# Kernel optimization log

Hardware: AMD Instinct MI355X
Metric: run time of the kernel (lower is better)

The kernel has to match this reference:

```python
import jax, jax.numpy as jnp
import numpy as np

B, S, HID, NH = 2, 2048, 2048, 16
HD = HID // NH  # 128


def setup_inputs() -> dict:
    key = jax.random.key(0)
    ks = jax.random.split(key, 6)
    xav = lambda k, shape: jax.random.uniform(k, shape, jnp.float32,
        -jnp.sqrt(6.0 / (shape[0] + shape[1])), jnp.sqrt(6.0 / (shape[0] + shape[1])))
    return {
        'hidden_state': jax.random.normal(ks[0], (B, S, HID), jnp.float32),
        'attention_mask': jnp.ones((B, 1, 1, S), jnp.int32),
        'Wq': xav(ks[1], (HID, HID)), 'bq': jnp.zeros((HID,), jnp.float32),
        'Wk': xav(ks[2], (HD, HID)),  'bk': jnp.zeros((HD,), jnp.float32),
        'Wv': xav(ks[3], (HD, HID)),  'bv': jnp.zeros((HD,), jnp.float32),
        'Wo': xav(ks[4], (HID, HID)), 'bo': jnp.zeros((HID,), jnp.float32),
    }


def reference(hidden_state, attention_mask, Wq, bq, Wk, bk, Wv, bv, Wo, bo):
    b, s, _ = hidden_state.shape
    scale = 1.0 / jnp.sqrt(jnp.float32(HD))
    # projections (torch Linear: y = x @ W.T + b)
    q = hidden_state @ Wq.T + bq                      # (B,S,HID)
    k = hidden_state @ Wk.T + bk                      # (B,S,HD) single KV head
    v = hidden_state @ Wv.T + bv                      # (B,S,HD)
    q = q.reshape(b, s, NH, HD).transpose(0, 2, 1, 3)  # (B,H,S,D)
    # scores with shared KV head broadcast over query heads
    scores = jnp.einsum('bhqd,bkd->bhqk', q, k) * scale  # (B,H,S,S)
    scores = jnp.where(attention_mask == 0, -jnp.inf, scores)
    probs = jax.nn.softmax(scores, axis=-1)
    out = jnp.einsum('bhqk,bkd->bhqd', probs, v)       # (B,H,S,D)
    out = out.transpose(0, 2, 1, 3).reshape(b, s, HID)
    return out @ Wo.T + bo
```

## Files before the change

kernel.cpp:

```cpp
#include <hip/hip_runtime.h>

#define B_   2
#define S_   2048
#define HID_ 2048
#define NH_  16
#define HD_  128
#define M_   (B_ * S_)

using half4   = __attribute__((ext_vector_type(4))) _Float16;
using half8   = __attribute__((ext_vector_type(8))) _Float16;
using floatx4 = __attribute__((ext_vector_type(4))) float;

__device__ __forceinline__ void gl_lds16(const void* g, void* l) {
  __builtin_amdgcn_global_load_lds(
      (const __attribute__((address_space(1))) void*)g,
      (__attribute__((address_space(3))) void*)l, 16, 0, 0);
}

__device__ __forceinline__ void cvt8(const float* s, _Float16* d, int i) {
  const floatx4* sp = (const floatx4*)s;
  floatx4 a = sp[(size_t)i * 2];
  floatx4 b = sp[(size_t)i * 2 + 1];
  half8 h;
  h[0] = (_Float16)a[0]; h[1] = (_Float16)a[1];
  h[2] = (_Float16)a[2]; h[3] = (_Float16)a[3];
  h[4] = (_Float16)b[0]; h[5] = (_Float16)b[1];
  h[6] = (_Float16)b[2]; h[7] = (_Float16)b[3];
  *(half8*)(d + (size_t)i * 8) = h;
}

__global__ __launch_bounds__(256) void cvt_all(
    const float* __restrict__ h,  const float* __restrict__ wq,
    const float* __restrict__ wk, const float* __restrict__ wv,
    const float* __restrict__ wo,
    _Float16* __restrict__ dh,  _Float16* __restrict__ dwq,
    _Float16* __restrict__ dwk, _Float16* __restrict__ dwv,
    _Float16* __restrict__ dwo) {
  int bid = blockIdx.x;
  const float* s;
  _Float16* d;
  int off;
  if (bid < 4096)      { s = h;  d = dh;  off = bid; }
  else if (bid < 6144) { s = wq; d = dwq; off = bid - 4096; }
  else if (bid < 6272) { s = wk; d = dwk; off = bid - 6144; }
  else if (bid < 6400) { s = wv; d = dwv; off = bid - 6272; }
  else                 { s = wo; d = dwo; off = bid - 6400; }
  cvt8(s, d, off * 256 + threadIdx.x);
}

template <typename OutT, bool TRANS>
__device__ __forceinline__ void gemm128_body(
    const _Float16* __restrict__ A, const _Float16* __restrict__ W,
    const float* __restrict__ bias, OutT* __restrict__ C,
    int Nout, int K, int m0, int n0w, int c0) {
  __shared__ __align__(16) _Float16 As[128][32];
  __shared__ __align__(16) _Float16 Ws[128][32];

  const int tid  = threadIdx.x;
  const int lane = tid & 63;
  const int wave = tid >> 6;
  const int wm   = wave >> 1, wn = wave & 1;
  const int l15  = lane & 15, lq = lane >> 4;
  const int srow = wave * 16 + (lane >> 2);
  const int scol = (lane & 3) * 8;

  floatx4 acc[4][4];
#pragma unroll
  for (int i = 0; i < 4; i++)
#pragma unroll
    for (int j = 0; j < 4; j++) acc[i][j] = (floatx4){0.f, 0.f, 0.f, 0.f};

  const _Float16* Ag = A + (size_t)(m0 + srow) * K + scol;
  const _Float16* Wg = W + (size_t)(n0w + srow) * K + scol;
  const size_t step64 = (size_t)64 * K;

  for (int kt = 0; kt < K; kt += 32) {
    gl_lds16(Ag + kt,          &As[wave * 16][0]);
    gl_lds16(Ag + step64 + kt, &As[64 + wave * 16][0]);
    gl_lds16(Wg + kt,          &Ws[wave * 16][0]);
    gl_lds16(Wg + step64 + kt, &Ws[64 + wave * 16][0]);
    __syncthreads();

    half8 af[4], bf[4];
#pragma unroll
    for (int i = 0; i < 4; i++)
      af[i] = *(const half8*)&As[wm * 64 + i * 16 + l15][lq * 8];
#pragma unroll
    for (int j = 0; j < 4; j++)
      bf[j] = *(const half8*)&Ws[wn * 64 + j * 16 + l15][lq * 8];
#pragma unroll
    for (int i = 0; i < 4; i++)
#pragma unroll
      for (int j = 0; j < 4; j++)
        acc[i][j] = __builtin_amdgcn_mfma_f32_16x16x32_f16(af[i], bf[j], acc[i][j], 0, 0, 0);
    __syncthreads();
  }

  const int rq = lq * 4;
  if constexpr (TRANS) {
    const int b  = m0 / S_;
    const int sb = m0 - b * S_ + wm * 64;
#pragma unroll
    for (int j = 0; j < 4; j++) {
      int col  = wn * 64 + j * 16 + l15;
      float bv = bias[n0w + col];
#pragma unroll
      for (int i = 0; i < 4; i++) {
        half4 o;
#pragma unroll
        for (int r = 0; r < 4; r++) o[r] = (_Float16)(acc[i][j][r] + bv);
        *(half4*)((_Float16*)C + (size_t)b * HD_ * S_ + (size_t)col * S_
                  + sb + i * 16 + rq) = o;
      }
    }
  } else {
#pragma unroll
    for (int j = 0; j < 4; j++) {
      int col_l = wn * 64 + j * 16 + l15;
      float bv  = bias[n0w + col_l];
#pragma unroll
      for (int i = 0; i < 4; i++) {
        int row = m0 + wm * 64 + i * 16 + rq;
#pragma unroll
        for (int r = 0; r < 4; r++)
          C[(size_t)(row + r) * Nout + c0 + col_l] = (OutT)(acc[i][j][r] + bv);
      }
    }
  }
}

__global__ __launch_bounds__(256) void gemm_qkv(
    const _Float16* __restrict__ A,
    const _Float16* __restrict__ Wq, const float* __restrict__ bq, _Float16* __restrict__ Qh,
    const _Float16* __restrict__ Wk, const float* __restrict__ bk, _Float16* __restrict__ Kh,
    const _Float16* __restrict__ Wv, const float* __restrict__ bv, _Float16* __restrict__ VhT) {
  const int nt = blockIdx.x, m0 = blockIdx.y * 128;
  if (nt < 16)
    gemm128_body<_Float16, false>(A, Wq, bq, Qh, HID_, HID_, m0, nt * 128, nt * 128);
  else if (nt == 16)
    gemm128_body<_Float16, false>(A, Wk, bk, Kh, HD_, HID_, m0, 0, 0);
  else
    gemm128_body<_Float16, true>(A, Wv, bv, VhT, HD_, HID_, m0, 0, 0);
}

__global__ __launch_bounds__(256) void gemm_out(
    const _Float16* __restrict__ A, const _Float16* __restrict__ W,
    const float* __restrict__ bias, float* __restrict__ C) {
  gemm128_body<float, false>(A, W, bias, C, HID_, HID_, blockIdx.y * 128,
                             blockIdx.x * 128, blockIdx.x * 128);
}

__global__ __launch_bounds__(256, 2) void attn_mfma(
    const _Float16* __restrict__ Q, const _Float16* __restrict__ K,
    const _Float16* __restrict__ VhT, const int* __restrict__ mask,
    _Float16* __restrict__ Obuf) {
  constexpr int BN = 64, KP = 136, VP = 72, NT = S_ / BN;
  __shared__ __align__(16) _Float16 Ks[2][BN][KP];
  __shared__ __align__(16) _Float16 Vt[2][HD_][VP];

  const int tid  = threadIdx.x;
  const int lane = tid & 63, wave = tid >> 6;
  const int l15  = lane & 15, lq = lane >> 4;
  const int q0   = blockIdx.x * 128;
  const int b    = blockIdx.y >> 4, h = blockIdx.y & 15;
  const float sl2e = 0.08838834764831845f * 1.44269504088896341f;
  const _Float16* VT = VhT + (size_t)b * HD_ * S_;
  const _Float16* Kb = K + (size_t)b * S_ * HD_;
  const int* mb = mask + b * S_;

  int krow[4], kcol[4], vrow[4], vcol[4];
#pragma unroll
  for (int it = 0; it < 4; it++) {
    int i = it * 256 + tid;
    krow[it] = i >> 4;  kcol[it] = (i & 15) * 8;
    vrow[it] = i >> 3;  vcol[it] = (i & 7) * 8;
  }

  half8 qf[2][4];
#pragma unroll
  for (int i = 0; i < 2; i++)
#pragma unroll
    for (int kd = 0; kd < 4; kd++)
      qf[i][kd] = *(const half8*)(Q + (size_t)(b * S_ + q0 + wave * 32 + i * 16 + l15) * HID_
                                  + h * HD_ + kd * 32 + lq * 8);

  float m_i[2] = {-3.0e38f, -3.0e38f};
  float l_p[2] = {0.f, 0.f};
  floatx4 oacc[2][8];
#pragma unroll
  for (int i = 0; i < 2; i++)
#pragma unroll
    for (int jd = 0; jd < 8; jd++) oacc[i][jd] = (floatx4){0.f, 0.f, 0.f, 0.f};

  half8 kreg[4], vreg[4];
#pragma unroll
  for (int it = 0; it < 4; it++) {
    kreg[it] = *(const half8*)(Kb + (size_t)krow[it] * HD_ + kcol[it]);
    vreg[it] = *(const half8*)(VT + (size_t)vrow[it] * S_ + vcol[it]);
  }
#pragma unroll
  for (int it = 0; it < 4; it++) {
    *(half8*)&Ks[0][krow[it]][kcol[it]] = kreg[it];
    *(half8*)&Vt[0][vrow[it]][vcol[it]] = vreg[it];
  }
  __syncthreads();

  for (int t = 0; t < NT; t++) {
    const int cur = t & 1;
    const int n0  = t * BN;
    const bool has_next = (t + 1) < NT;

    if (has_next) {
      const int nn = n0 + BN;
#pragma unroll
      for (int it = 0; it < 4; it++) {
        kreg[it] = *(const half8*)(Kb + (size_t)(nn + krow[it]) * HD_ + kcol[it]);
        vreg[it] = *(const half8*)(VT + (size_t)vrow[it] * S_ + nn + vcol[it]);
      }
    }

    int4 mk4[4];
#pragma unroll
    for (int j = 0; j < 4; j++)
      mk4[j] = *(const int4*)(mb + n0 + j * 16 + lq * 4);

    floatx4 st[4][2];
#pragma unroll
    for (int j = 0; j < 4; j++)
#pragma unroll
      for (int i = 0; i < 2; i++) st[j][i] = (floatx4){0.f, 0.f, 0.f, 0.f};
#pragma unroll
    for (int kd = 0; kd < 4; kd++) {
      half8 kb[4];
#pragma unroll
      for (int j = 0; j < 4; j++)
        kb[j] = *(const half8*)&Ks[cur][j * 16 + l15][kd * 32 + lq * 8];
#pragma unroll
      for (int j = 0; j < 4; j++)
#pragma unroll
        for (int i = 0; i < 2; i++)
          st[j][i] = __builtin_amdgcn_mfma_f32_16x16x32_f16(kb[j], qf[i][kd], st[j][i], 0, 0, 0);
    }

    floatx4 amf[4];
#pragma unroll
    for (int j = 0; j < 4; j++) {
      amf[j][0] = mk4[j].x ? 0.f : -3.0e38f;
      amf[j][1] = mk4[j].y ? 0.f : -3.0e38f;
      amf[j][2] = mk4[j].z ? 0.f : -3.0e38f;
      amf[j][3] = mk4[j].w ? 0.f : -3.0e38f;
    }

    half4 ph[2][4];
#pragma unroll
    for (int i = 0; i < 2; i++) {
      float mx = -3.0e38f;
#pragma unroll
      for (int j = 0; j < 4; j++)
#pragma unroll
        for (int r = 0; r < 4; r++) {
          float v = st[j][i][r] * sl2e + amf[j][r];
          st[j][i][r] = v;
          mx = fmaxf(mx, v);
        }
      mx = fmaxf(mx, __shfl_xor(mx, 16));
      mx = fmaxf(mx, __shfl_xor(mx, 32));
      float mnew  = fmaxf(m_i[i], mx);
      float alpha = __builtin_amdgcn_exp2f(m_i[i] - mnew);
      m_i[i] = mnew;
      float rs = 0.f;
#pragma unroll
      for (int j = 0; j < 4; j++)
#pragma unroll
        for (int r = 0; r < 4; r++) {
          float pv = __builtin_amdgcn_exp2f(st[j][i][r] - mnew);
          ph[i][j][r] = (_Float16)pv;
          rs += pv;
        }
      l_p[i] = l_p[i] * alpha + rs;
      if (__any(alpha < 1.0f)) {
#pragma unroll
        for (int r = 0; r < 4; r++) {
          float a_r = __shfl(alpha, lq * 4 + r);
#pragma unroll
          for (int jd = 0; jd < 8; jd++) oacc[i][jd][r] *= a_r;
        }
      }
    }

#pragma unroll
    for (int j = 0; j < 4; j++) {
#pragma unroll
      for (int jd = 0; jd < 8; jd++) {
        half4 vb = *(const half4*)&Vt[cur][jd * 16 + l15][j * 16 + lq * 4];
#pragma unroll
        for (int i = 0; i < 2; i++)
          oacc[i][jd] = __builtin_amdgcn_mfma_f32_16x16x16f16(ph[i][j], vb, oacc[i][jd], 0, 0, 0);
      }
    }

    if (has_next) {
      const int nxt = 1 - cur;
#pragma unroll
      for (int it = 0; it < 4; it++) {
        *(half8*)&Ks[nxt][krow[it]][kcol[it]] = kreg[it];
        *(half8*)&Vt[nxt][vrow[it]][vcol[it]] = vreg[it];
      }
    }
    __syncthreads();
  }

#pragma unroll
  for (int i = 0; i < 2; i++) {
    float l = l_p[i];
    l += __shfl_xor(l, 16);
    l += __shfl_xor(l, 32);
    float linv = 1.0f / l;
#pragma unroll
    for (int r = 0; r < 4; r++) {
      float lr = __shfl(linv, lq * 4 + r);
      size_t row = (size_t)(b * S_ + q0 + wave * 32 + i * 16 + lq * 4 + r);
#pragma unroll
      for (int jd = 0; jd < 8; jd++)
        Obuf[row * HID_ + h * HD_ + jd * 16 + l15] = (_Float16)(oacc[i][jd][r] * lr);
    }
  }
}

extern "C" void kernel_launch(void* const* d_in, const int* in_sizes, int n_in,
                              void* d_out, int out_size, void* d_ws, size_t ws_size,
                              hipStream_t stream) {
  const float* hidden = (const float*)d_in[0];
  const int*   mask   = (const int*)d_in[1];
  const float* Wq = (const float*)d_in[2];
  const float* bq = (const float*)d_in[3];
  const float* Wk = (const float*)d_in[4];
  const float* bk = (const float*)d_in[5];
  const float* Wv = (const float*)d_in[6];
  const float* bv = (const float*)d_in[7];
  const float* Wo = (const float*)d_in[8];
  const float* bo = (const float*)d_in[9];
  float* out = (float*)d_out;

  char* p = (char*)d_ws;
  auto alloc = [&](size_t bytes) {
    char* r = p;
    p += (bytes + 255) & ~(size_t)255;
    return r;
  };
  _Float16* hidh  = (_Float16*)alloc((size_t)M_ * HID_ * 2);
  _Float16* Wqh   = (_Float16*)alloc((size_t)HID_ * HID_ * 2);
  _Float16* Wkh   = (_Float16*)alloc((size_t)HD_ * HID_ * 2);
  _Float16* Wvh   = (_Float16*)alloc((size_t)HD_ * HID_ * 2);
  _Float16* Woh   = (_Float16*)alloc((size_t)HID_ * HID_ * 2);
  _Float16* Qh    = (_Float16*)alloc((size_t)M_ * HID_ * 2);
  _Float16* Kh    = (_Float16*)alloc((size_t)M_ * HD_ * 2);
  _Float16* VhT   = (_Float16*)alloc((size_t)M_ * HD_ * 2);
  _Float16* attnh = (_Float16*)alloc((size_t)M_ * HID_ * 2);

  cvt_all<<<8448, 256, 0, stream>>>(hidden, Wq, Wk, Wv, Wo,
                                    hidh, Wqh, Wkh, Wvh, Woh);

  dim3 gqkv(18, M_ / 128);
  gemm_qkv<<<gqkv, 256, 0, stream>>>(hidh, Wqh, bq, Qh, Wkh, bk, Kh, Wvh, bv, VhT);

  dim3 ga(S_ / 128, B_ * NH_);
  attn_mfma<<<ga, 256, 0, stream>>>(Qh, Kh, VhT, mask, attnh);

  dim3 go(HID_ / 128, M_ / 128);
  gemm_out<<<go, 256, 0, stream>>>(attnh, Woh, bo, out);
}
```

Before: 325.5 us.

## Split KV tile across waves in attention, halve query tile, lazy softmax rescale

The attention block now covers 64 queries instead of 128. Its four waves form two query groups times two key halves, so each wave processes 32 of the 64 keys in every tile. The two partial softmax states (running max, running sum and output accumulator) are merged at the end through LDS reused from the K/V buffers, and the grid doubles. The online-softmax rescale is also made lazy: it runs only when some row's new max exceeds the old one by more than 8 in log2 units. The aim is more blocks and fewer rescale operations, at the cost of twice the K/V tile loads per query, half the MFMA work per barrier, and an extra merge pass.

```diff
diff --git a/kernel.cpp b/kernel.cpp
--- a/kernel.cpp
+++ b/kernel.cpp
@@ -160,8 +160,10 @@
 
   const int tid  = threadIdx.x;
   const int lane = tid & 63, wave = tid >> 6;
+  const int qg   = wave & 1;
+  const int kvh  = wave >> 1;
   const int l15  = lane & 15, lq = lane >> 4;
-  const int q0   = blockIdx.x * 128;
+  const int q0   = blockIdx.x * 64;
   const int b    = blockIdx.y >> 4, h = blockIdx.y & 15;
   const float sl2e = 0.08838834764831845f * 1.44269504088896341f;
   const _Float16* VT = VhT + (size_t)b * HD_ * S_;
@@ -181,7 +183,7 @@
   for (int i = 0; i < 2; i++)
 #pragma unroll
     for (int kd = 0; kd < 4; kd++)
-      qf[i][kd] = *(const half8*)(Q + (size_t)(b * S_ + q0 + wave * 32 + i * 16 + l15) * HID_
+      qf[i][kd] = *(const half8*)(Q + (size_t)(b * S_ + q0 + qg * 32 + i * 16 + l15) * HID_
                                   + h * HD_ + kd * 32 + lq * 8);
 
   float m_i[2] = {-3.0e38f, -3.0e38f};
@@ -207,11 +209,11 @@
 
   for (int t = 0; t < NT; t++) {
     const int cur = t & 1;
-    const int n0  = t * BN;
+    const int nw  = t * BN + kvh * 32;
     const bool has_next = (t + 1) < NT;
 
     if (has_next) {
-      const int nn = n0 + BN;
+      const int nn = (t + 1) * BN;
 #pragma unroll
       for (int it = 0; it < 4; it++) {
         kreg[it] = *(const half8*)(Kb + (size_t)(nn + krow[it]) * HD_ + kcol[it]);
@@ -219,44 +221,44 @@
       }
     }
 
-    int4 mk4[4];
-#pragma unroll
-    for (int j = 0; j < 4; j++)
-      mk4[j] = *(const int4*)(mb + n0 + j * 16 + lq * 4);
-
-    floatx4 st[4][2];
-#pragma unroll
-    for (int j = 0; j < 4; j++)
+    int4 mk4[2];
+#pragma unroll
+    for (int j = 0; j < 2; j++)
+      mk4[j] = *(const int4*)(mb + nw + j * 16 + lq * 4);
+
+    floatx4 st[2][2];
+#pragma unroll
+    for (int j = 0; j < 2; j++)
 #pragma unroll
       for (int i = 0; i < 2; i++) st[j][i] = (floatx4){0.f, 0.f, 0.f, 0.f};
 #pragma unroll
     for (int kd = 0; kd < 4; kd++) {
-      half8 kb[4];
-#pragma unroll
-      for (int j = 0; j < 4; j++)
-        kb[j] = *(const half8*)&Ks[cur][j * 16 + l15][kd * 32 + lq * 8];
-#pragma unroll
-      for (int j = 0; j < 4; j++)
+      half8 kb[2];
+#pragma unroll
+      for (int j = 0; j < 2; j++)
+        kb[j] = *(const half8*)&Ks[cur][kvh * 32 + j * 16 + l15][kd * 32 + lq * 8];
+#pragma unroll
+      for (int j = 0; j < 2; j++)
 #pragma unroll
         for (int i = 0; i < 2; i++)
           st[j][i] = __builtin_amdgcn_mfma_f32_16x16x32_f16(kb[j], qf[i][kd], st[j][i], 0, 0, 0);
     }
 
-    floatx4 amf[4];
-#pragma unroll
-    for (int j = 0; j < 4; j++) {
+    floatx4 amf[2];
+#pragma unroll
+    for (int j = 0; j < 2; j++) {
       amf[j][0] = mk4[j].x ? 0.f : -3.0e38f;
       amf[j][1] = mk4[j].y ? 0.f : -3.0e38f;
       amf[j][2] = mk4[j].z ? 0.f : -3.0e38f;
       amf[j][3] = mk4[j].w ? 0.f : -3.0e38f;
     }
 
-    half4 ph[2][4];
+    half4 ph[2][2];
 #pragma unroll
     for (int i = 0; i < 2; i++) {
       float mx = -3.0e38f;
 #pragma unroll
-      for (int j = 0; j < 4; j++)
+      for (int j = 0; j < 2; j++)
 #pragma unroll
         for (int r = 0; r < 4; r++) {
           float v = st[j][i][r] * sl2e + amf[j][r];
@@ -265,34 +267,35 @@
         }
       mx = fmaxf(mx, __shfl_xor(mx, 16));
       mx = fmaxf(mx, __shfl_xor(mx, 32));
-      float mnew  = fmaxf(m_i[i], mx);
-      float alpha = __builtin_amdgcn_exp2f(m_i[i] - mnew);
-      m_i[i] = mnew;
+      if (!__all(mx <= m_i[i] + 8.0f)) {
+        float mnew  = fmaxf(m_i[i], mx);
+        float alpha = __builtin_amdgcn_exp2f(m_i[i] - mnew);
+        m_i[i] = mnew;
+        l_p[i] *= alpha;
+#pragma unroll
+        for (int r = 0; r < 4; r++) {
+          float a_r = __shfl(alpha, lq * 4 + r);
+#pragma unroll
+          for (int jd = 0; jd < 8; jd++) oacc[i][jd][r] *= a_r;
+        }
+      }
       float rs = 0.f;
 #pragma unroll
-      for (int j = 0; j < 4; j++)
+      for (int j = 0; j < 2; j++)
 #pragma unroll
         for (int r = 0; r < 4; r++) {
-          float pv = __builtin_amdgcn_exp2f(st[j][i][r] - mnew);
+          float pv = __builtin_amdgcn_exp2f(st[j][i][r] - m_i[i]);
           ph[i][j][r] = (_Float16)pv;
           rs += pv;
         }
-      l_p[i] = l_p[i] * alpha + rs;
-      if (__any(alpha < 1.0f)) {
-#pragma unroll
-        for (int r = 0; r < 4; r++) {
-          float a_r = __shfl(alpha, lq * 4 + r);
-#pragma unroll
-          for (int jd = 0; jd < 8; jd++) oacc[i][jd][r] *= a_r;
-        }
-      }
-    }
-
-#pragma unroll
-    for (int j = 0; j < 4; j++) {
+      l_p[i] += rs;
+    }
+
+#pragma unroll
+    for (int j = 0; j < 2; j++) {
 #pragma unroll
       for (int jd = 0; jd < 8; jd++) {
-        half4 vb = *(const half4*)&Vt[cur][jd * 16 + l15][j * 16 + lq * 4];
+        half4 vb = *(const half4*)&Vt[cur][jd * 16 + l15][kvh * 32 + j * 16 + lq * 4];
 #pragma unroll
         for (int i = 0; i < 2; i++)
           oacc[i][jd] = __builtin_amdgcn_mfma_f32_16x16x16f16(ph[i][j], vb, oacc[i][jd], 0, 0, 0);
@@ -310,19 +313,60 @@
     __syncthreads();
   }
 
+  float lw[2];
 #pragma unroll
   for (int i = 0; i < 2; i++) {
     float l = l_p[i];
     l += __shfl_xor(l, 16);
     l += __shfl_xor(l, 32);
-    float linv = 1.0f / l;
-#pragma unroll
-    for (int r = 0; r < 4; r++) {
-      float lr = __shfl(linv, lq * 4 + r);
-      size_t row = (size_t)(b * S_ + q0 + wave * 32 + i * 16 + lq * 4 + r);
+    lw[i] = l;
+  }
+
+  __syncthreads();
+  float* Osc = (float*)&Ks[0][0][0];
+  float* MLs = (float*)&Vt[0][0][0];
+
+  if (kvh == 1) {
+    if (lq == 0) {
+#pragma unroll
+      for (int i = 0; i < 2; i++) {
+        MLs[((qg * 2 + i) * 2 + 0) * 16 + l15] = m_i[i];
+        MLs[((qg * 2 + i) * 2 + 1) * 16 + l15] = lw[i];
+      }
+    }
+#pragma unroll
+    for (int i = 0; i < 2; i++)
 #pragma unroll
       for (int jd = 0; jd < 8; jd++)
-        Obuf[row * HID_ + h * HD_ + jd * 16 + l15] = (_Float16)(oacc[i][jd][r] * lr);
+#pragma unroll
+        for (int r = 0; r < 4; r++)
+          Osc[(qg * 32 + i * 16 + lq * 4 + r) * 129 + jd * 16 + l15] = oacc[i][jd][r];
+  }
+  __syncthreads();
+
+  if (kvh == 0) {
+#pragma unroll
+    for (int i = 0; i < 2; i++) {
+      float m1 = m_i[i];
+      float m2 = MLs[((qg * 2 + i) * 2 + 0) * 16 + l15];
+      float l2 = MLs[((qg * 2 + i) * 2 + 1) * 16 + l15];
+      float mn = fmaxf(m1, m2);
+      float a1 = __builtin_amdgcn_exp2f(m1 - mn);
+      float a2 = __builtin_amdgcn_exp2f(m2 - mn);
+      float linv = 1.0f / (lw[i] * a1 + l2 * a2);
+      float s1v = a1 * linv, s2v = a2 * linv;
+#pragma unroll
+      for (int r = 0; r < 4; r++) {
+        float s1 = __shfl(s1v, lq * 4 + r);
+        float s2 = __shfl(s2v, lq * 4 + r);
+        size_t row = (size_t)(b * S_ + q0 + qg * 32 + i * 16 + lq * 4 + r);
+#pragma unroll
+        for (int jd = 0; jd < 8; jd++) {
+          float o2 = Osc[(qg * 32 + i * 16 + lq * 4 + r) * 129 + jd * 16 + l15];
+          Obuf[row * HID_ + h * HD_ + jd * 16 + l15] =
+              (_Float16)(oacc[i][jd][r] * s1 + o2 * s2);
+        }
+      }
     }
   }
 }
@@ -364,7 +408,7 @@
   dim3 gqkv(18, M_ / 128);
   gemm_qkv<<<gqkv, 256, 0, stream>>>(hidh, Wqh, bq, Qh, Wkh, bk, Kh, Wvh, bv, VhT);
 
-  dim3 ga(S_ / 128, B_ * NH_);
+  dim3 ga(S_ / 64, B_ * NH_);
   attn_mfma<<<ga, 256, 0, stream>>>(Qh, Kh, VhT, mask, attnh);
 
   dim3 go(HID_ / 128, M_ / 128);
```

Measured after the change: 336.3 us. 1.03x slower.

## Double-buffer GEMM LDS tiles and add lazy softmax max rescaling in attention

Applied to the files above, without the earlier changes.

The projection GEMM now uses two LDS buffers for A and W, so the next K-tile's global-to-LDS copy can be issued before the MFMAs on the current tile. This is meant to hide load latency, at the cost of doubled LDS per block and a loop that assumes K is a multiple of 64. Separately, the flash-attention online softmax now updates the running max and rescales the accumulator only when some row's new max exceeds the old one by more than 8 (in log2 units). This skips most rescale passes but lets probabilities reach up to 2^8 before the fp16 conversion, which risks precision or overflow.

```diff
diff --git a/kernel.cpp b/kernel.cpp
--- a/kernel.cpp
+++ b/kernel.cpp
@@ -53,8 +53,10 @@
     const _Float16* __restrict__ A, const _Float16* __restrict__ W,
     const float* __restrict__ bias, OutT* __restrict__ C,
     int Nout, int K, int m0, int n0w, int c0) {
-  __shared__ __align__(16) _Float16 As[128][32];
-  __shared__ __align__(16) _Float16 Ws[128][32];
+  __shared__ __align__(16) _Float16 As0[128][32];
+  __shared__ __align__(16) _Float16 As1[128][32];
+  __shared__ __align__(16) _Float16 Ws0[128][32];
+  __shared__ __align__(16) _Float16 Ws1[128][32];
 
   const int tid  = threadIdx.x;
   const int lane = tid & 63;
@@ -74,25 +76,36 @@
   const _Float16* Wg = W + (size_t)(n0w + srow) * K + scol;
   const size_t step64 = (size_t)64 * K;
 
-  for (int kt = 0; kt < K; kt += 32) {
-    gl_lds16(Ag + kt,          &As[wave * 16][0]);
-    gl_lds16(Ag + step64 + kt, &As[64 + wave * 16][0]);
-    gl_lds16(Wg + kt,          &Ws[wave * 16][0]);
-    gl_lds16(Wg + step64 + kt, &Ws[64 + wave * 16][0]);
+  auto stage = [&](_Float16 (*Asb)[32], _Float16 (*Wsb)[32], int kt2) {
+    gl_lds16(Ag + kt2,          &Asb[wave * 16][0]);
+    gl_lds16(Ag + step64 + kt2, &Asb[64 + wave * 16][0]);
+    gl_lds16(Wg + kt2,          &Wsb[wave * 16][0]);
+    gl_lds16(Wg + step64 + kt2, &Wsb[64 + wave * 16][0]);
+  };
+  auto compute = [&](const _Float16 (*Asb)[32], const _Float16 (*Wsb)[32]) {
+    half8 af[4], bf[4];
+#pragma unroll
+    for (int i = 0; i < 4; i++)
+      af[i] = *(const half8*)&Asb[wm * 64 + i * 16 + l15][lq * 8];
+#pragma unroll
+    for (int j = 0; j < 4; j++)
+      bf[j] = *(const half8*)&Wsb[wn * 64 + j * 16 + l15][lq * 8];
+#pragma unroll
+    for (int i = 0; i < 4; i++)
+#pragma unroll
+      for (int j = 0; j < 4; j++)
+        acc[i][j] = __builtin_amdgcn_mfma_f32_16x16x32_f16(af[i], bf[j], acc[i][j], 0, 0, 0);
+  };
+
+  stage(As0, Ws0, 0);
+  __syncthreads();
+
+  for (int kt = 0; kt < K; kt += 64) {
+    stage(As1, Ws1, kt + 32);
+    compute(As0, Ws0);
     __syncthreads();
-
-    half8 af[4], bf[4];
-#pragma unroll
-    for (int i = 0; i < 4; i++)
-      af[i] = *(const half8*)&As[wm * 64 + i * 16 + l15][lq * 8];
-#pragma unroll
-    for (int j = 0; j < 4; j++)
-      bf[j] = *(const half8*)&Ws[wn * 64 + j * 16 + l15][lq * 8];
-#pragma unroll
-    for (int i = 0; i < 4; i++)
-#pragma unroll
-      for (int j = 0; j < 4; j++)
-        acc[i][j] = __builtin_amdgcn_mfma_f32_16x16x32_f16(af[i], bf[j], acc[i][j], 0, 0, 0);
+    if (kt + 64 < K) stage(As0, Ws0, kt + 64);
+    compute(As1, Ws1);
     __syncthreads();
   }
 
@@ -265,27 +278,28 @@
         }
       mx = fmaxf(mx, __shfl_xor(mx, 16));
       mx = fmaxf(mx, __shfl_xor(mx, 32));
-      float mnew  = fmaxf(m_i[i], mx);
-      float alpha = __builtin_amdgcn_exp2f(m_i[i] - mnew);
-      m_i[i] = mnew;
+      if (!__all(mx <= m_i[i] + 8.0f)) {
+        float mnew  = fmaxf(m_i[i], mx);
+        float alpha = __builtin_amdgcn_exp2f(m_i[i] - mnew);
+        m_i[i] = mnew;
+        l_p[i] *= alpha;
+#pragma unroll
+        for (int r = 0; r < 4; r++) {
+          float a_r = __shfl(alpha, lq * 4 + r);
+#pragma unroll
+          for (int jd = 0; jd < 8; jd++) oacc[i][jd][r] *= a_r;
+        }
+      }
       float rs = 0.f;
 #pragma unroll
       for (int j = 0; j < 4; j++)
 #pragma unroll
         for (int r = 0; r < 4; r++) {
-          float pv = __builtin_amdgcn_exp2f(st[j][i][r] - mnew);
+          float pv = __builtin_amdgcn_exp2f(st[j][i][r] - m_i[i]);
           ph[i][j][r] = (_Float16)pv;
           rs += pv;
         }
-      l_p[i] = l_p[i] * alpha + rs;
-      if (__any(alpha < 1.0f)) {
-#pragma unroll
-        for (int r = 0; r < 4; r++) {
-          float a_r = __shfl(alpha, lq * 4 + r);
-#pragma unroll
-          for (int jd = 0; jd < 8; jd++) oacc[i][jd][r] *= a_r;
-        }
-      }
+      l_p[i] += rs;
     }
 
 #pragma unroll
```

Measured after the change: 333.8 us. 2.6% more time.

## Use 128x256 double-buffered GEMM tiles and lazy softmax rescaling in attention

Applied to the files above, without the earlier changes.

The projection and output GEMMs move from 128x128 single-buffered tiles to 128x256 tiles run by 512 threads. They use a BK=64 double-buffered LDS pipeline, so the next tile's global-to-LDS load overlaps the MFMA work. K and V projections now share one block. The attention softmax only rescales the running max and accumulators when the new max exceeds the old one by more than 8 in log2 units, which skips most rescale passes. This uses more LDS per block, which may lower occupancy, and it lets unnormalised probabilities grow up to 2^8 in fp16.

```diff
diff --git a/kernel.cpp b/kernel.cpp
--- a/kernel.cpp
+++ b/kernel.cpp
@@ -48,21 +48,30 @@
   cvt8(s, d, off * 256 + threadIdx.x);
 }
 
-template <typename OutT, bool TRANS>
-__device__ __forceinline__ void gemm128_body(
-    const _Float16* __restrict__ A, const _Float16* __restrict__ W,
-    const float* __restrict__ bias, OutT* __restrict__ C,
-    int Nout, int K, int m0, int n0w, int c0) {
-  __shared__ __align__(16) _Float16 As[128][32];
-  __shared__ __align__(16) _Float16 Ws[128][32];
-
+struct GemmSmem {
+  _Float16 As[2][2][128][32];
+  _Float16 Bs[2][2][256][32];
+};
+
+template <int MODE, typename OutT>
+__device__ __forceinline__ void gemm256_body(
+    GemmSmem* sm,
+    const _Float16* __restrict__ A,
+    const _Float16* __restrict__ W0,
+    const _Float16* __restrict__ W1,
+    const float* __restrict__ biasA,
+    const float* __restrict__ biasB,
+    OutT* __restrict__ C, _Float16* __restrict__ CT,
+    int Nout, int m0, int c0) {
   const int tid  = threadIdx.x;
   const int lane = tid & 63;
   const int wave = tid >> 6;
-  const int wm   = wave >> 1, wn = wave & 1;
+  const int wm   = wave >> 2;
+  const int wn   = wave & 3;
   const int l15  = lane & 15, lq = lane >> 4;
-  const int srow = wave * 16 + (lane >> 2);
-  const int scol = (lane & 3) * 8;
+  const int srow = tid >> 2;
+  const int scol = (tid & 3) * 8;
+  const int wrow = wave * 16;
 
   floatx4 acc[4][4];
 #pragma unroll
@@ -70,84 +79,99 @@
 #pragma unroll
     for (int j = 0; j < 4; j++) acc[i][j] = (floatx4){0.f, 0.f, 0.f, 0.f};
 
-  const _Float16* Ag = A + (size_t)(m0 + srow) * K + scol;
-  const _Float16* Wg = W + (size_t)(n0w + srow) * K + scol;
-  const size_t step64 = (size_t)64 * K;
-
-  for (int kt = 0; kt < K; kt += 32) {
-    gl_lds16(Ag + kt,          &As[wave * 16][0]);
-    gl_lds16(Ag + step64 + kt, &As[64 + wave * 16][0]);
-    gl_lds16(Wg + kt,          &Ws[wave * 16][0]);
-    gl_lds16(Wg + step64 + kt, &Ws[64 + wave * 16][0]);
+  const _Float16* Ag  = A  + (size_t)(m0 + srow) * HID_ + scol;
+  const _Float16* W0g = W0 + (size_t)srow * HID_ + scol;
+  const _Float16* W1g = W1 + (size_t)srow * HID_ + scol;
+
+  auto stage = [&](int bufi, int kt) {
+#pragma unroll
+    for (int s = 0; s < 2; s++) {
+      gl_lds16(Ag  + kt + s * 32, &sm->As[bufi][s][wrow][0]);
+      gl_lds16(W0g + kt + s * 32, &sm->Bs[bufi][s][wrow][0]);
+      gl_lds16(W1g + kt + s * 32, &sm->Bs[bufi][s][128 + wrow][0]);
+    }
+  };
+  auto compute = [&](int bufi) {
+#pragma unroll
+    for (int s = 0; s < 2; s++) {
+      half8 af[4], bf[4];
+#pragma unroll
+      for (int i = 0; i < 4; i++)
+        af[i] = *(const half8*)&sm->As[bufi][s][wm * 64 + i * 16 + l15][lq * 8];
+#pragma unroll
+      for (int j = 0; j < 4; j++)
+        bf[j] = *(const half8*)&sm->Bs[bufi][s][wn * 64 + j * 16 + l15][lq * 8];
+#pragma unroll
+      for (int i = 0; i < 4; i++)
+#pragma unroll
+        for (int j = 0; j < 4; j++)
+          acc[i][j] = __builtin_amdgcn_mfma_f32_16x16x32_f16(af[i], bf[j], acc[i][j], 0, 0, 0);
+    }
+  };
+
+  stage(0, 0);
+  __syncthreads();
+  int bufi = 0;
+  for (int kt = 0; kt < HID_; kt += 64) {
+    if (kt + 64 < HID_) stage(bufi ^ 1, kt + 64);
+    compute(bufi);
     __syncthreads();
-
-    half8 af[4], bf[4];
-#pragma unroll
-    for (int i = 0; i < 4; i++)
-      af[i] = *(const half8*)&As[wm * 64 + i * 16 + l15][lq * 8];
-#pragma unroll
-    for (int j = 0; j < 4; j++)
-      bf[j] = *(const half8*)&Ws[wn * 64 + j * 16 + l15][lq * 8];
-#pragma unroll
-    for (int i = 0; i < 4; i++)
-#pragma unroll
-      for (int j = 0; j < 4; j++)
-        acc[i][j] = __builtin_amdgcn_mfma_f32_16x16x32_f16(af[i], bf[j], acc[i][j], 0, 0, 0);
-    __syncthreads();
+    bufi ^= 1;
   }
 
   const int rq = lq * 4;
-  if constexpr (TRANS) {
-    const int b  = m0 / S_;
-    const int sb = m0 - b * S_ + wm * 64;
-#pragma unroll
-    for (int j = 0; j < 4; j++) {
-      int col  = wn * 64 + j * 16 + l15;
-      float bv = bias[n0w + col];
+#pragma unroll
+  for (int j = 0; j < 4; j++) {
+    const int colt = wn * 64 + j * 16 + l15;
+    if (MODE != 1 || colt < 128) {
+      float bv = (colt < 128) ? biasA[colt] : biasB[colt - 128];
+#pragma unroll
+      for (int i = 0; i < 4; i++) {
+        int row = m0 + wm * 64 + i * 16 + rq;
+#pragma unroll
+        for (int r = 0; r < 4; r++)
+          C[(size_t)(row + r) * Nout + c0 + colt] = (OutT)(acc[i][j][r] + bv);
+      }
+    } else {
+      const int colv = colt - 128;
+      float bv = biasB[colv];
+      const int bb = m0 / S_;
+      const int sb = m0 - bb * S_ + wm * 64;
 #pragma unroll
       for (int i = 0; i < 4; i++) {
         half4 o;
 #pragma unroll
         for (int r = 0; r < 4; r++) o[r] = (_Float16)(acc[i][j][r] + bv);
-        *(half4*)((_Float16*)C + (size_t)b * HD_ * S_ + (size_t)col * S_
+        *(half4*)(CT + (size_t)bb * HD_ * S_ + (size_t)colv * S_
                   + sb + i * 16 + rq) = o;
       }
     }
-  } else {
-#pragma unroll
-    for (int j = 0; j < 4; j++) {
-      int col_l = wn * 64 + j * 16 + l15;
-      float bv  = bias[n0w + col_l];
-#pragma unroll
-      for (int i = 0; i < 4; i++) {
-        int row = m0 + wm * 64 + i * 16 + rq;
-#pragma unroll
-        for (int r = 0; r < 4; r++)
-          C[(size_t)(row + r) * Nout + c0 + col_l] = (OutT)(acc[i][j][r] + bv);
-      }
-    }
-  }
-}
-
-__global__ __launch_bounds__(256) void gemm_qkv(
+  }
+}
+
+__global__ __launch_bounds__(512, 2) void gemm_qkv(
     const _Float16* __restrict__ A,
     const _Float16* __restrict__ Wq, const float* __restrict__ bq, _Float16* __restrict__ Qh,
     const _Float16* __restrict__ Wk, const float* __restrict__ bk, _Float16* __restrict__ Kh,
     const _Float16* __restrict__ Wv, const float* __restrict__ bv, _Float16* __restrict__ VhT) {
+  __shared__ __align__(16) GemmSmem sm;
   const int nt = blockIdx.x, m0 = blockIdx.y * 128;
-  if (nt < 16)
-    gemm128_body<_Float16, false>(A, Wq, bq, Qh, HID_, HID_, m0, nt * 128, nt * 128);
-  else if (nt == 16)
-    gemm128_body<_Float16, false>(A, Wk, bk, Kh, HD_, HID_, m0, 0, 0);
+  if (nt < 8)
+    gemm256_body<0, _Float16>(&sm, A, Wq + (size_t)nt * 256 * HID_,
+                              Wq + (size_t)(nt * 256 + 128) * HID_,
+                              bq + nt * 256, bq + nt * 256 + 128,
+                              Qh, nullptr, HID_, m0, nt * 256);
   else
-    gemm128_body<_Float16, true>(A, Wv, bv, VhT, HD_, HID_, m0, 0, 0);
-}
-
-__global__ __launch_bounds__(256) void gemm_out(
+    gemm256_body<1, _Float16>(&sm, A, Wk, Wv, bk, bv, Kh, VhT, HD_, m0, 0);
+}
+
+__global__ __launch_bounds__(512, 2) void gemm_out(
     const _Float16* __restrict__ A, const _Float16* __restrict__ W,
     const float* __restrict__ bias, float* __restrict__ C) {
-  gemm128_body<float, false>(A, W, bias, C, HID_, HID_, blockIdx.y * 128,
-                             blockIdx.x * 128, blockIdx.x * 128);
+  __shared__ __align__(16) GemmSmem sm;
+  const int n0 = blockIdx.x * 256, m0 = blockIdx.y * 128;
+  gemm256_body<2, float>(&sm, A, W + (size_t)n0 * HID_, W + (size_t)(n0 + 128) * HID_,
+                         bias + n0, bias + n0 + 128, C, nullptr, HID_, m0, n0);
 }
 
 __global__ __launch_bounds__(256, 2) void attn_mfma(
@@ -265,27 +289,28 @@
         }
       mx = fmaxf(mx, __shfl_xor(mx, 16));
       mx = fmaxf(mx, __shfl_xor(mx, 32));
-      float mnew  = fmaxf(m_i[i], mx);
-      float alpha = __builtin_amdgcn_exp2f(m_i[i] - mnew);
-      m_i[i] = mnew;
+      if (!__all(mx <= m_i[i] + 8.0f)) {
+        float mnew  = fmaxf(m_i[i], mx);
+        float alpha = __builtin_amdgcn_exp2f(m_i[i] - mnew);
+        m_i[i] = mnew;
+        l_p[i] *= alpha;
+#pragma unroll
+        for (int r = 0; r < 4; r++) {
+          float a_r = __shfl(alpha, lq * 4 + r);
+#pragma unroll
+          for (int jd = 0; jd < 8; jd++) oacc[i][jd][r] *= a_r;
+        }
+      }
       float rs = 0.f;
 #pragma unroll
       for (int j = 0; j < 4; j++)
 #pragma unroll
         for (int r = 0; r < 4; r++) {
-          float pv = __builtin_amdgcn_exp2f(st[j][i][r] - mnew);
+          float pv = __builtin_amdgcn_exp2f(st[j][i][r] - m_i[i]);
           ph[i][j][r] = (_Float16)pv;
           rs += pv;
         }
-      l_p[i] = l_p[i] * alpha + rs;
-      if (__any(alpha < 1.0f)) {
-#pragma unroll
-        for (int r = 0; r < 4; r++) {
-          float a_r = __shfl(alpha, lq * 4 + r);
-#pragma unroll
-          for (int jd = 0; jd < 8; jd++) oacc[i][jd][r] *= a_r;
-        }
-      }
+      l_p[i] += rs;
     }
 
 #pragma unroll
@@ -361,12 +386,12 @@
   cvt_all<<<8448, 256, 0, stream>>>(hidden, Wq, Wk, Wv, Wo,
                                     hidh, Wqh, Wkh, Wvh, Woh);
 
-  dim3 gqkv(18, M_ / 128);
-  gemm_qkv<<<gqkv, 256, 0, stream>>>(hidh, Wqh, bq, Qh, Wkh, bk, Kh, Wvh, bv, VhT);
+  dim3 gqkv(9, M_ / 128);
+  gemm_qkv<<<gqkv, 512, 0, stream>>>(hidh, Wqh, bq, Qh, Wkh, bk, Kh, Wvh, bv, VhT);
 
   dim3 ga(S_ / 128, B_ * NH_);
   attn_mfma<<<ga, 256, 0, stream>>>(Qh, Kh, VhT, mask, attnh);
 
-  dim3 go(HID_ / 128, M_ / 128);
-  gemm_out<<<go, 256, 0, stream>>>(attnh, Woh, bo, out);
-}
+  dim3 go(HID_ / 256, M_ / 128);
+  gemm_out<<<go, 512, 0, stream>>>(attnh, Woh, bo, out);
+}
```

After: 335.3 us. 3.0% more time.
